# Kernel optimization log

Measured on AMD Instinct MI355X. Metric: run time of the kernel, lower is better.

## Reference

```python
import jax, jax.numpy as jnp
import numpy as np

N = 50000
E = 600000
D = 128
BN_EPS = 1e-5
GIN_EPS = 0.0  # init_eps=0, not learned


def setup_inputs() -> dict:
    key = jax.random.key(0)
    ks = jax.random.split(key, 8)
    x = jax.random.normal(ks[0], (N, D), dtype=jnp.float32)
    edge_index = jax.random.randint(ks[1], (2, E), 0, N, dtype=jnp.int64)
    s = 1.0 / np.sqrt(D)
    w1 = jax.random.uniform(ks[2], (D, D), jnp.float32, -s, s)
    b1 = jax.random.uniform(ks[3], (D,), jnp.float32, -s, s)
    w2 = jax.random.uniform(ks[4], (D, D), jnp.float32, -s, s)
    b2 = jax.random.uniform(ks[5], (D,), jnp.float32, -s, s)
    gamma = jnp.ones((D,), jnp.float32)
    beta = jnp.zeros((D,), jnp.float32)
    return {"x": x, "edge_index": edge_index, "w1": w1, "b1": b1,
            "w2": w2, "b2": b2, "gamma": gamma, "beta": beta}


def reference(x, edge_index, w1, b1, w2, b2, gamma, beta):
    src, dst = edge_index[0], edge_index[1]
    # GINConv sum aggregation: out[i] = sum_{(j,i) in E} x[j]
    agg = jax.ops.segment_sum(x[src], dst, num_segments=N)  # [N, D]
    h = (1.0 + GIN_EPS) * x + agg
    # 2-layer MLP (Linear-ReLU-Linear)
    h = jax.nn.relu(h @ w1 + b1)
    h = h @ w2 + b2
    # training-mode BatchNorm over nodes (biased variance)
    mean = jnp.mean(h, axis=0)
    var = jnp.var(h, axis=0)
    h = (h - mean) * jax.lax.rsqrt(var + BN_EPS) * gamma + beta
    h = jax.nn.relu(h)
    # residual (in_dim == out_dim); dropout p=0.0 -> identity
    return x + h
```

## Files before the change

kernel.cpp:

```cpp
#include <hip/hip_runtime.h>

#define NN 50000
#define EE 600000
#define DD 128
#define MAXDEG 64
#define NSLICE 32
#define RST 136
#define UNITS (NN / 16)

typedef __attribute__((ext_vector_type(8))) short short8;
typedef __attribute__((ext_vector_type(4))) float f32x4;

static __device__ __forceinline__ unsigned short f2bf(float f) {
    unsigned int u = __float_as_uint(f);
    u += 0x7FFF + ((u >> 16) & 1);
    return (unsigned short)(u >> 16);
}
static __device__ __forceinline__ float bflo(unsigned int u) {
    return __uint_as_float(u << 16);
}
static __device__ __forceinline__ float bfhi(unsigned int u) {
    return __uint_as_float(u & 0xFFFF0000u);
}


__global__ __launch_bounds__(256) void k_prep(const float* __restrict__ w1,
                                              const float* __restrict__ w2,
                                              const float* __restrict__ x,
                                              const int* __restrict__ ei,
                                              int* __restrict__ cursor,
                                              unsigned short* __restrict__ srcPad,
                                              unsigned short* __restrict__ wt,
                                              unsigned int* __restrict__ xb) {
    int tid = blockIdx.x * 256 + threadIdx.x;
    if (tid < EE) {
        int s = ei[tid];
        int d = ei[EE + tid];
        int pos = atomicAdd(&cursor[d], 1);
        if (pos < MAXDEG) srcPad[(d << 6) + pos] = (unsigned short)s;
    }
    if (tid < 32768) {
        int w = tid >> 14, idx = tid & 16383;
        int k = idx >> 7, n = idx & 127;
        const float* src = w ? w2 : w1;
        wt[w * 16384 + n * 128 + k] = f2bf(src[k * 128 + n]);
    }
    int xi = tid - 32768;
    if (xi >= 0 && xi < NN * DD / 4) {
        float4 v = ((const float4*)x)[xi];
        uint2 p;
        p.x = (unsigned int)f2bf(v.x) | ((unsigned int)f2bf(v.y) << 16);
        p.y = (unsigned int)f2bf(v.z) | ((unsigned int)f2bf(v.w) << 16);
        ((uint2*)xb)[xi] = p;
    }
}


__global__ __launch_bounds__(256) void k_fused(const unsigned int* __restrict__ xb,
                                               const int* __restrict__ cursor,
                                               const unsigned short* __restrict__ srcPad,
                                               const unsigned short* __restrict__ wt,
                                               const float* __restrict__ b1,
                                               const float* __restrict__ b2,
                                               unsigned short* __restrict__ h2b,
                                               float* __restrict__ priv) {
    __shared__ __align__(16) unsigned short tile[16 * RST];
    int w    = threadIdx.x >> 6;
    int lane = threadIdx.x & 63;
    int unit = blockIdx.x;
    int base = unit * 16;
    int m = lane & 15, quad = lane >> 4;

    int ct4[4], sv4[4];
    unsigned int self4[4];
    #pragma unroll
    for (int i = 0; i < 4; ++i) {
        int node = base + w * 4 + i;
        ct4[i]   = cursor[node];
        sv4[i]   = srcPad[(node << 6) + lane];
        self4[i] = xb[(node << 6) + lane];
    }
    #pragma unroll
    for (int i = 0; i < 4; ++i) {
        int cnt = ct4[i] > MAXDEG ? MAXDEG : ct4[i];
        int sv = sv4[i];
        float ax = bflo(self4[i]), ay = bfhi(self4[i]);
        {
            unsigned int buf[16];
            #pragma unroll
            for (int j = 0; j < 16; ++j) {
                int a = __shfl(sv, j, 64);
                buf[j] = (j < cnt) ? xb[(a << 6) + lane] : 0u;
            }
            #pragma unroll
            for (int j = 0; j < 16; ++j) { ax += bflo(buf[j]); ay += bfhi(buf[j]); }
        }
        if (cnt > 16) {
            unsigned int buf[16];
            #pragma unroll
            for (int j = 0; j < 16; ++j) {
                int a = __shfl(sv, 16 + j, 64);
                buf[j] = (16 + j < cnt) ? xb[(a << 6) + lane] : 0u;
            }
            #pragma unroll
            for (int j = 0; j < 16; ++j) { ax += bflo(buf[j]); ay += bfhi(buf[j]); }
            for (int j = 32; j < cnt; ++j) {
                int s = __shfl(sv, j, 64);
                unsigned int u = xb[(s << 6) + lane];
                ax += bflo(u);
                ay += bfhi(u);
            }
        }
        ((unsigned int*)(tile + (w * 4 + i) * RST))[lane] =
            (unsigned int)f2bf(ax) | ((unsigned int)f2bf(ay) << 16);
    }
    __syncthreads();

    short8 af[4];
    #pragma unroll
    for (int kc = 0; kc < 4; ++kc)
        af[kc] = *(const short8*)&tile[m * RST + kc * 32 + quad * 8];
    __syncthreads();
    {
        short8 wf[2][4];
        #pragma unroll
        for (int t = 0; t < 2; ++t)
            #pragma unroll
            for (int kc = 0; kc < 4; ++kc)
                wf[t][kc] = *(const short8*)&wt[((w * 2 + t) * 16 + m) * 128 + kc * 32 + quad * 8];
        f32x4 acc[2];
        acc[0] = (f32x4)0.f; acc[1] = (f32x4)0.f;
        #pragma unroll
        for (int kc = 0; kc < 4; ++kc)
            #pragma unroll
            for (int t = 0; t < 2; ++t)
                acc[t] = __builtin_amdgcn_mfma_f32_16x16x32_bf16(af[kc], wf[t][kc], acc[t], 0, 0, 0);
        #pragma unroll
        for (int t = 0; t < 2; ++t) {
            int col = (w * 2 + t) * 16 + m;
            float bv = b1[col];
            #pragma unroll
            for (int r = 0; r < 4; ++r)
                tile[(quad * 4 + r) * RST + col] = f2bf(fmaxf(acc[t][r] + bv, 0.f));
        }
    }
    __syncthreads();

    #pragma unroll
    for (int kc = 0; kc < 4; ++kc)
        af[kc] = *(const short8*)&tile[m * RST + kc * 32 + quad * 8];
    {
        const unsigned short* W2t = wt + 16384;
        short8 wf[2][4];
        #pragma unroll
        for (int t = 0; t < 2; ++t)
            #pragma unroll
            for (int kc = 0; kc < 4; ++kc)
                wf[t][kc] = *(const short8*)&W2t[((w * 2 + t) * 16 + m) * 128 + kc * 32 + quad * 8];
        f32x4 acc[2];
        acc[0] = (f32x4)0.f; acc[1] = (f32x4)0.f;
        #pragma unroll
        for (int kc = 0; kc < 4; ++kc)
            #pragma unroll
            for (int t = 0; t < 2; ++t)
                acc[t] = __builtin_amdgcn_mfma_f32_16x16x32_bf16(af[kc], wf[t][kc], acc[t], 0, 0, 0);
        float* myslice = priv + (unit & (NSLICE - 1)) * 2 * DD;
        #pragma unroll
        for (int t = 0; t < 2; ++t) {
            int col = (w * 2 + t) * 16 + m;
            float bv = b2[col];
            float s = 0.f, sq = 0.f;
            #pragma unroll
            for (int r = 0; r < 4; ++r) {
                float v = acc[t][r] + bv;
                h2b[(base + quad * 4 + r) * 128 + col] = f2bf(v);
                s += v;
                sq += v * v;
            }
            s  += __shfl_down(s, 32, 64);  sq += __shfl_down(sq, 32, 64);
            s  += __shfl_down(s, 16, 64);  sq += __shfl_down(sq, 16, 64);
            if (quad == 0) {
                atomicAdd(&myslice[col], s);
                atomicAdd(&myslice[DD + col], sq);
            }
        }
    }
}


__global__ __launch_bounds__(256) void k_final(const float* __restrict__ x,
                                               const unsigned int* __restrict__ h2,
                                               float* __restrict__ out,
                                               const float* __restrict__ priv,
                                               const float* __restrict__ gamma,
                                               const float* __restrict__ beta) {
    __shared__ float ssc[DD], ssh[DD];
    int t = threadIdx.x;
    if (t < DD) {
        float s = 0.f, sq = 0.f;
        #pragma unroll
        for (int sl = 0; sl < NSLICE; ++sl) {
            s  += priv[sl * 2 * DD + t];
            sq += priv[sl * 2 * DD + DD + t];
        }
        float mean = s * (1.0f / NN);
        float var = fmaxf(sq * (1.0f / NN) - mean * mean, 0.f);
        float sc = gamma[t] * rsqrtf(var + 1e-5f);
        ssc[t] = sc;
        ssh[t] = beta[t] - mean * sc;
    }
    __syncthreads();
    #pragma unroll
    for (int u = 0; u < 4; ++u) {
        int idx = blockIdx.x * 1024 + u * 256 + t;
        if (idx >= NN * DD / 4) return;
        int c0 = (idx & 31) * 4;
        unsigned int p0 = h2[2 * idx];
        unsigned int p1 = h2[2 * idx + 1];
        float4 xv = ((const float4*)x)[idx];
        float4 o;
        o.x = xv.x + fmaxf(fmaf(bflo(p0), ssc[c0 + 0], ssh[c0 + 0]), 0.f);
        o.y = xv.y + fmaxf(fmaf(bfhi(p0), ssc[c0 + 1], ssh[c0 + 1]), 0.f);
        o.z = xv.z + fmaxf(fmaf(bflo(p1), ssc[c0 + 2], ssh[c0 + 2]), 0.f);
        o.w = xv.w + fmaxf(fmaf(bfhi(p1), ssc[c0 + 3], ssh[c0 + 3]), 0.f);
        ((float4*)out)[idx] = o;
    }
}

extern "C" void kernel_launch(void* const* d_in, const int* in_sizes, int n_in,
                              void* d_out, int out_size, void* d_ws, size_t ws_size,
                              hipStream_t stream) {
    (void)in_sizes; (void)n_in; (void)out_size; (void)ws_size;
    const float* x     = (const float*)d_in[0];
    const int*   ei    = (const int*)d_in[1];
    const float* w1    = (const float*)d_in[2];
    const float* b1    = (const float*)d_in[3];
    const float* w2    = (const float*)d_in[4];
    const float* b2    = (const float*)d_in[5];
    const float* gamma = (const float*)d_in[6];
    const float* beta  = (const float*)d_in[7];
    float* out = (float*)d_out;
    char* wsb  = (char*)d_ws;

    int*            cursor = (int*)wsb;
    float*          priv   = (float*)(wsb + 0x31000);
    unsigned short* srcPad = (unsigned short*)(wsb + 0x40000);
    unsigned int*   xb     = (unsigned int*)(wsb + 0x680000);
    unsigned int*   h2w    = (unsigned int*)(wsb + 0x2C00000);
    unsigned short* wt     = (unsigned short*)(wsb + 0x3880000);
    unsigned short* h2b    = (unsigned short*)h2w;

    (void)hipMemsetAsync(wsb, 0, 0x39000, stream);

    k_prep <<<(32768 + NN * DD / 4 + 255) / 256, 256, 0, stream>>>(w1, w2, x, ei, cursor, srcPad, wt, xb);
    k_fused<<<UNITS, 256, 0, stream>>>(xb, cursor, srcPad, wt, b1, b2, h2b, priv);
    k_final<<<(NN * DD / 4 + 1023) / 1024, 256, 0, stream>>>(x, h2w, out, priv, gamma, beta);
}
```

Before: 173.1 us.

## Make fused GIN kernel persistent with atomic work queue and paired-node gathers

```diff
diff --git a/kernel.cpp b/kernel.cpp
--- a/kernel.cpp
+++ b/kernel.cpp
@@ -7,6 +7,7 @@
 #define NSLICE 32
 #define RST 136
 #define UNITS (NN / 16)
+#define NBLK 2048
 
 typedef __attribute__((ext_vector_type(8))) short short8;
 typedef __attribute__((ext_vector_type(4))) float f32x4;
@@ -56,132 +57,166 @@
 }
 
 
-__global__ __launch_bounds__(256) void k_fused(const unsigned int* __restrict__ xb,
-                                               const int* __restrict__ cursor,
-                                               const unsigned short* __restrict__ srcPad,
-                                               const unsigned short* __restrict__ wt,
-                                               const float* __restrict__ b1,
-                                               const float* __restrict__ b2,
-                                               unsigned short* __restrict__ h2b,
-                                               float* __restrict__ priv) {
+__global__ __launch_bounds__(256, 8) void k_fused(const unsigned int* __restrict__ xb,
+                                                  const int* __restrict__ cursor,
+                                                  const unsigned short* __restrict__ srcPad,
+                                                  const unsigned short* __restrict__ wt,
+                                                  const float* __restrict__ b1,
+                                                  const float* __restrict__ b2,
+                                                  unsigned short* __restrict__ h2b,
+                                                  float* __restrict__ priv,
+                                                  int* __restrict__ unit_ctr) {
     __shared__ __align__(16) unsigned short tile[16 * RST];
+    __shared__ int s_unit;
     int w    = threadIdx.x >> 6;
     int lane = threadIdx.x & 63;
-    int unit = blockIdx.x;
-    int base = unit * 16;
     int m = lane & 15, quad = lane >> 4;
 
-    int ct4[4], sv4[4];
-    unsigned int self4[4];
-    #pragma unroll
-    for (int i = 0; i < 4; ++i) {
-        int node = base + w * 4 + i;
-        ct4[i]   = cursor[node];
-        sv4[i]   = srcPad[(node << 6) + lane];
-        self4[i] = xb[(node << 6) + lane];
-    }
-    #pragma unroll
-    for (int i = 0; i < 4; ++i) {
-        int cnt = ct4[i] > MAXDEG ? MAXDEG : ct4[i];
-        int sv = sv4[i];
-        float ax = bflo(self4[i]), ay = bfhi(self4[i]);
+    for (;;) {
+        if (threadIdx.x == 0) s_unit = atomicAdd(unit_ctr, 1);
+        __syncthreads();
+        int unit = s_unit;
+        if (unit >= UNITS) return;
+        int base = unit * 16;
+
+        int ct4[4], sv4[4];
+        unsigned int self4[4];
+        #pragma unroll
+        for (int i = 0; i < 4; ++i) {
+            int node = base + w * 4 + i;
+            ct4[i]   = cursor[node];
+            sv4[i]   = srcPad[(node << 6) + lane];
+            self4[i] = xb[(node << 6) + lane];
+        }
+        #pragma unroll
+        for (int p = 0; p < 2; ++p) {
+            int cnt0 = ct4[2 * p]     > MAXDEG ? MAXDEG : ct4[2 * p];
+            int cnt1 = ct4[2 * p + 1] > MAXDEG ? MAXDEG : ct4[2 * p + 1];
+            int sv0 = sv4[2 * p], sv1 = sv4[2 * p + 1];
+            float ax0 = bflo(self4[2 * p]),     ay0 = bfhi(self4[2 * p]);
+            float ax1 = bflo(self4[2 * p + 1]), ay1 = bfhi(self4[2 * p + 1]);
+            {
+                unsigned int buf0[16], buf1[16];
+                #pragma unroll
+                for (int j = 0; j < 16; ++j) {
+                    int a0 = __shfl(sv0, j, 64);
+                    buf0[j] = (j < cnt0) ? xb[(a0 << 6) + lane] : 0u;
+                }
+                #pragma unroll
+                for (int j = 0; j < 16; ++j) {
+                    int a1 = __shfl(sv1, j, 64);
+                    buf1[j] = (j < cnt1) ? xb[(a1 << 6) + lane] : 0u;
+                }
+                #pragma unroll
+                for (int j = 0; j < 16; ++j) {
+                    ax0 += bflo(buf0[j]); ay0 += bfhi(buf0[j]);
+                    ax1 += bflo(buf1[j]); ay1 += bfhi(buf1[j]);
+                }
+            }
+            if (cnt0 > 16) {
+                unsigned int buf[16];
+                #pragma unroll
+                for (int j = 0; j < 16; ++j) {
+                    int a = __shfl(sv0, 16 + j, 64);
+                    buf[j] = (16 + j < cnt0) ? xb[(a << 6) + lane] : 0u;
+                }
+                #pragma unroll
+                for (int j = 0; j < 16; ++j) { ax0 += bflo(buf[j]); ay0 += bfhi(buf[j]); }
+                for (int j = 32; j < cnt0; ++j) {
+                    int s = __shfl(sv0, j, 64);
+                    unsigned int u = xb[(s << 6) + lane];
+                    ax0 += bflo(u); ay0 += bfhi(u);
+                }
+            }
+            if (cnt1 > 16) {
+                unsigned int buf[16];
+                #pragma unroll
+                for (int j = 0; j < 16; ++j) {
+                    int a = __shfl(sv1, 16 + j, 64);
+                    buf[j] = (16 + j < cnt1) ? xb[(a << 6) + lane] : 0u;
+                }
+                #pragma unroll
+                for (int j = 0; j < 16; ++j) { ax1 += bflo(buf[j]); ay1 += bfhi(buf[j]); }
+                for (int j = 32; j < cnt1; ++j) {
+                    int s = __shfl(sv1, j, 64);
+                    unsigned int u = xb[(s << 6) + lane];
+                    ax1 += bflo(u); ay1 += bfhi(u);
+                }
+            }
+            ((unsigned int*)(tile + (w * 4 + 2 * p) * RST))[lane] =
+                (unsigned int)f2bf(ax0) | ((unsigned int)f2bf(ay0) << 16);
+            ((unsigned int*)(tile + (w * 4 + 2 * p + 1) * RST))[lane] =
+                (unsigned int)f2bf(ax1) | ((unsigned int)f2bf(ay1) << 16);
+        }
+        __syncthreads();
+
+        short8 af[4];
+        #pragma unroll
+        for (int kc = 0; kc < 4; ++kc)
+            af[kc] = *(const short8*)&tile[m * RST + kc * 32 + quad * 8];
+        __syncthreads();
         {
-            unsigned int buf[16];
-            #pragma unroll
-            for (int j = 0; j < 16; ++j) {
-                int a = __shfl(sv, j, 64);
-                buf[j] = (j < cnt) ? xb[(a << 6) + lane] : 0u;
-            }
-            #pragma unroll
-            for (int j = 0; j < 16; ++j) { ax += bflo(buf[j]); ay += bfhi(buf[j]); }
-        }
-        if (cnt > 16) {
-            unsigned int buf[16];
-            #pragma unroll
-            for (int j = 0; j < 16; ++j) {
-                int a = __shfl(sv, 16 + j, 64);
-                buf[j] = (16 + j < cnt) ? xb[(a << 6) + lane] : 0u;
-            }
-            #pragma unroll
-            for (int j = 0; j < 16; ++j) { ax += bflo(buf[j]); ay += bfhi(buf[j]); }
-            for (int j = 32; j < cnt; ++j) {
-                int s = __shfl(sv, j, 64);
-                unsigned int u = xb[(s << 6) + lane];
-                ax += bflo(u);
-                ay += bfhi(u);
-            }
-        }
-        ((unsigned int*)(tile + (w * 4 + i) * RST))[lane] =
-            (unsigned int)f2bf(ax) | ((unsigned int)f2bf(ay) << 16);
-    }
-    __syncthreads();
-
-    short8 af[4];
-    #pragma unroll
-    for (int kc = 0; kc < 4; ++kc)
-        af[kc] = *(const short8*)&tile[m * RST + kc * 32 + quad * 8];
-    __syncthreads();
-    {
-        short8 wf[2][4];
-        #pragma unroll
-        for (int t = 0; t < 2; ++t)
+            short8 wf[2][4];
+            #pragma unroll
+            for (int t = 0; t < 2; ++t)
+                #pragma unroll
+                for (int kc = 0; kc < 4; ++kc)
+                    wf[t][kc] = *(const short8*)&wt[((w * 2 + t) * 16 + m) * 128 + kc * 32 + quad * 8];
+            f32x4 acc[2];
+            acc[0] = (f32x4)0.f; acc[1] = (f32x4)0.f;
             #pragma unroll
             for (int kc = 0; kc < 4; ++kc)
-                wf[t][kc] = *(const short8*)&wt[((w * 2 + t) * 16 + m) * 128 + kc * 32 + quad * 8];
-        f32x4 acc[2];
-        acc[0] = (f32x4)0.f; acc[1] = (f32x4)0.f;
+                #pragma unroll
+                for (int t = 0; t < 2; ++t)
+                    acc[t] = __builtin_amdgcn_mfma_f32_16x16x32_bf16(af[kc], wf[t][kc], acc[t], 0, 0, 0);
+            #pragma unroll
+            for (int t = 0; t < 2; ++t) {
+                int col = (w * 2 + t) * 16 + m;
+                float bv = b1[col];
+                #pragma unroll
+                for (int r = 0; r < 4; ++r)
+                    tile[(quad * 4 + r) * RST + col] = f2bf(fmaxf(acc[t][r] + bv, 0.f));
+            }
+        }
+        __syncthreads();
+
         #pragma unroll
         for (int kc = 0; kc < 4; ++kc)
+            af[kc] = *(const short8*)&tile[m * RST + kc * 32 + quad * 8];
+        {
+            const unsigned short* W2t = wt + 16384;
+            short8 wf[2][4];
             #pragma unroll
             for (int t = 0; t < 2; ++t)
-                acc[t] = __builtin_amdgcn_mfma_f32_16x16x32_bf16(af[kc], wf[t][kc], acc[t], 0, 0, 0);
-        #pragma unroll
-        for (int t = 0; t < 2; ++t) {
-            int col = (w * 2 + t) * 16 + m;
-            float bv = b1[col];
-            #pragma unroll
-            for (int r = 0; r < 4; ++r)
-                tile[(quad * 4 + r) * RST + col] = f2bf(fmaxf(acc[t][r] + bv, 0.f));
-        }
-    }
-    __syncthreads();
-
-    #pragma unroll
-    for (int kc = 0; kc < 4; ++kc)
-        af[kc] = *(const short8*)&tile[m * RST + kc * 32 + quad * 8];
-    {
-        const unsigned short* W2t = wt + 16384;
-        short8 wf[2][4];
-        #pragma unroll
-        for (int t = 0; t < 2; ++t)
+                #pragma unroll
+                for (int kc = 0; kc < 4; ++kc)
+                    wf[t][kc] = *(const short8*)&W2t[((w * 2 + t) * 16 + m) * 128 + kc * 32 + quad * 8];
+            f32x4 acc[2];
+            acc[0] = (f32x4)0.f; acc[1] = (f32x4)0.f;
             #pragma unroll
             for (int kc = 0; kc < 4; ++kc)
-                wf[t][kc] = *(const short8*)&W2t[((w * 2 + t) * 16 + m) * 128 + kc * 32 + quad * 8];
-        f32x4 acc[2];
-        acc[0] = (f32x4)0.f; acc[1] = (f32x4)0.f;
-        #pragma unroll
-        for (int kc = 0; kc < 4; ++kc)
-            #pragma unroll
-            for (int t = 0; t < 2; ++t)
-                acc[t] = __builtin_amdgcn_mfma_f32_16x16x32_bf16(af[kc], wf[t][kc], acc[t], 0, 0, 0);
-        float* myslice = priv + (unit & (NSLICE - 1)) * 2 * DD;
-        #pragma unroll
-        for (int t = 0; t < 2; ++t) {
-            int col = (w * 2 + t) * 16 + m;
-            float bv = b2[col];
-            float s = 0.f, sq = 0.f;
-            #pragma unroll
-            for (int r = 0; r < 4; ++r) {
-                float v = acc[t][r] + bv;
-                h2b[(base + quad * 4 + r) * 128 + col] = f2bf(v);
-                s += v;
-                sq += v * v;
-            }
-            s  += __shfl_down(s, 32, 64);  sq += __shfl_down(sq, 32, 64);
-            s  += __shfl_down(s, 16, 64);  sq += __shfl_down(sq, 16, 64);
-            if (quad == 0) {
-                atomicAdd(&myslice[col], s);
-                atomicAdd(&myslice[DD + col], sq);
+                #pragma unroll
+                for (int t = 0; t < 2; ++t)
+                    acc[t] = __builtin_amdgcn_mfma_f32_16x16x32_bf16(af[kc], wf[t][kc], acc[t], 0, 0, 0);
+            float* myslice = priv + (unit & (NSLICE - 1)) * 2 * DD;
+            #pragma unroll
+            for (int t = 0; t < 2; ++t) {
+                int col = (w * 2 + t) * 16 + m;
+                float bv = b2[col];
+                float s = 0.f, sq = 0.f;
+                #pragma unroll
+                for (int r = 0; r < 4; ++r) {
+                    float v = acc[t][r] + bv;
+                    h2b[(base + quad * 4 + r) * 128 + col] = f2bf(v);
+                    s += v;
+                    sq += v * v;
+                }
+                s  += __shfl_down(s, 32, 64);  sq += __shfl_down(sq, 32, 64);
+                s  += __shfl_down(s, 16, 64);  sq += __shfl_down(sq, 16, 64);
+                if (quad == 0) {
+                    atomicAdd(&myslice[col], s);
+                    atomicAdd(&myslice[DD + col], sq);
+                }
             }
         }
     }
@@ -243,6 +278,7 @@
     char* wsb  = (char*)d_ws;
 
     int*            cursor = (int*)wsb;
+    int*            unit_ctr = (int*)(wsb + 0x30E00);
     float*          priv   = (float*)(wsb + 0x31000);
     unsigned short* srcPad = (unsigned short*)(wsb + 0x40000);
     unsigned int*   xb     = (unsigned int*)(wsb + 0x680000);
@@ -253,6 +289,6 @@
     (void)hipMemsetAsync(wsb, 0, 0x39000, stream);
 
     k_prep <<<(32768 + NN * DD / 4 + 255) / 256, 256, 0, stream>>>(w1, w2, x, ei, cursor, srcPad, wt, xb);
-    k_fused<<<UNITS, 256, 0, stream>>>(xb, cursor, srcPad, wt, b1, b2, h2b, priv);
+    k_fused<<<NBLK, 256, 0, stream>>>(xb, cursor, srcPad, wt, b1, b2, h2b, priv, unit_ctr);
     k_final<<<(NN * DD / 4 + 1023) / 1024, 256, 0, stream>>>(x, h2w, out, priv, gamma, beta);
 }
```

After: 222.8 us. +28.7%, slower.
